# Kernel tuning notes

Measured on AMD Instinct MI355X. Metric: run time of the kernel, lower is better.

The kernel has to match this reference:

```python
import jax, jax.numpy as jnp
import numpy as np

N_HEAD = 16


def setup_inputs() -> dict:
    key = jax.random.key(0)
    ks = jax.random.split(key, 5)
    B, S, D = 4, 2048, 1024
    scale = 1.0 / np.sqrt(D)
    return {
        "x": jax.random.normal(ks[0], (B, S, D), dtype=jnp.float32),
        "Wq": jax.random.normal(ks[1], (D, D), dtype=jnp.float32) * scale,
        "bq": jnp.zeros((D,), dtype=jnp.float32),
        "Wk": jax.random.normal(ks[2], (D, D), dtype=jnp.float32) * scale,
        "bk": jnp.zeros((D,), dtype=jnp.float32),
        "Wv": jax.random.normal(ks[3], (D, D), dtype=jnp.float32) * scale,
        "bv": jnp.zeros((D,), dtype=jnp.float32),
        "Wo": jax.random.normal(ks[4], (D, D), dtype=jnp.float32) * scale,
        "bo": jnp.zeros((D,), dtype=jnp.float32),
    }


def reference(x, Wq, bq, Wk, bk, Wv, bv, Wo, bo):
    B, S, D = x.shape
    H = N_HEAD
    Dh = D // H
    # projections (torch Linear == x @ W^T + b; here W stored as (in, out))
    q = (x @ Wq + bq).reshape(B, S, H, Dh).transpose(0, 2, 1, 3)  # (B,H,S,Dh)
    k = (x @ Wk + bk).reshape(B, S, H, Dh).transpose(0, 2, 1, 3)
    v = (x @ Wv + bv).reshape(B, S, H, Dh).transpose(0, 2, 1, 3)
    scores = jnp.einsum("bhsd,bhtd->bhst", q, k) / jnp.sqrt(jnp.float32(Dh))
    causal = jnp.tril(jnp.ones((S, S), dtype=bool))  # (S,S)
    scores = jnp.where(causal[None, None], scores, -jnp.inf)
    weights = jax.nn.softmax(scores, axis=-1)  # (B,H,S,S)
    attn = jnp.einsum("bhst,bhtd->bhsd", weights, v)
    attn = attn.transpose(0, 2, 1, 3).reshape(B, S, D)
    out = attn @ Wo + bo
    return out
```

## Files before the change

kernel.cpp:

```cpp
#include <hip/hip_runtime.h>
#include <hip/hip_bf16.h>


typedef __bf16 bf16x8 __attribute__((ext_vector_type(8)));
typedef float f32x4 __attribute__((ext_vector_type(4)));
typedef unsigned short u16;

__device__ __forceinline__ u16 f2b(float f) {
    __hip_bfloat16 h = __float2bfloat16(f);
    return __builtin_bit_cast(unsigned short, h);
}

__device__ __forceinline__ f32x4 mfma16(bf16x8 a, bf16x8 b, f32x4 c) {
    return __builtin_amdgcn_mfma_f32_16x16x32_bf16(a, b, c, 0, 0, 0);
}

typedef const __attribute__((address_space(1))) unsigned int* gas1_t;
typedef __attribute__((address_space(3))) unsigned int* las3_t;
__device__ __forceinline__ void gld16(const void* g, void* l) {
    __builtin_amdgcn_global_load_lds((gas1_t)g, (las3_t)l, 16, 0, 0);
}

__global__ __launch_bounds__(256) void convert_x(const float* __restrict__ x,
                                                 u16* __restrict__ xb, int n4) {
    int i = blockIdx.x * 256 + threadIdx.x;
    if (i < n4) {
        float4 v = ((const float4*)x)[i];
        ushort4 u;
        u.x = f2b(v.x); u.y = f2b(v.y); u.z = f2b(v.z); u.w = f2b(v.w);
        ((ushort4*)xb)[i] = u;
    }
}

__global__ __launch_bounds__(256) void transpose_w(const float* __restrict__ Wq,
                                                   const float* __restrict__ Wk,
                                                   const float* __restrict__ Wv,
                                                   const float* __restrict__ Wo,
                                                   u16* __restrict__ wqkvt,
                                                   u16* __restrict__ wot) {
    const int z = blockIdx.z;
    const float* src = (z == 0) ? Wq : (z == 1) ? Wk : (z == 2) ? Wv : Wo;
    u16* dst = (z == 3) ? wot : (wqkvt + (size_t)z * 1024 * 1024);
    __shared__ float tile[32][33];
    const int tx = threadIdx.x, ty = threadIdx.y;
    const int nbase = blockIdx.x * 32, kbase = blockIdx.y * 32;
    for (int j = 0; j < 4; ++j)
        tile[ty + j * 8][tx] = src[(size_t)(kbase + ty + j * 8) * 1024 + nbase + tx];
    __syncthreads();
    for (int j = 0; j < 4; ++j)
        dst[(size_t)(nbase + ty + j * 8) * 1024 + kbase + tx] = f2b(tile[tx][ty + j * 8]);
}

__global__ __launch_bounds__(256) void pack_bqkv(const float* __restrict__ bq,
                                                 const float* __restrict__ bk,
                                                 const float* __restrict__ bv,
                                                 float* __restrict__ bqkv) {
    int i = blockIdx.x * 256 + threadIdx.x;
    bqkv[i] = (i < 1024) ? bq[i] : (i < 2048) ? bk[i - 1024] : bv[i - 2048];
}

template <int MODE>
__global__ __launch_bounds__(256) void gemm_bt(const u16* __restrict__ A,
                                               const u16* __restrict__ Bt,
                                               const float* __restrict__ bias,
                                               void* __restrict__ Cout,
                                               void* __restrict__ Cout2,
                                               int M, int N, int K, int ldc) {
    const int tid = threadIdx.x;
    const int l = tid & 63;
    const int w = tid >> 6;
    const int tileM = blockIdx.x * 128;
    const int tileN = blockIdx.y * 128;

    __shared__ u16 As[128 * 32];
    __shared__ u16 Bs[128 * 32];

    const int srow = l >> 2;
    const int schunk = l & 3;
    const int mrow = l & 15;
    const int g8 = (l >> 4) * 8;
    const int waveM = (w & 1) * 64;
    const int waveN = (w >> 1) * 64;

    f32x4 acc[4][4] = {};

    for (int k0 = 0; k0 < K; k0 += 32) {
        gld16(A + (size_t)(tileM + w * 32 + srow) * K + k0 + schunk * 8, &As[(w * 2) * 512]);
        gld16(A + (size_t)(tileM + w * 32 + 16 + srow) * K + k0 + schunk * 8, &As[(w * 2 + 1) * 512]);
        gld16(Bt + (size_t)(tileN + w * 32 + srow) * K + k0 + schunk * 8, &Bs[(w * 2) * 512]);
        gld16(Bt + (size_t)(tileN + w * 32 + 16 + srow) * K + k0 + schunk * 8, &Bs[(w * 2 + 1) * 512]);
        __syncthreads();

        bf16x8 af[4], bf[4];
        for (int im = 0; im < 4; ++im)
            af[im] = *(const bf16x8*)&As[(waveM + im * 16 + mrow) * 32 + g8];
        for (int in = 0; in < 4; ++in)
            bf[in] = *(const bf16x8*)&Bs[(waveN + in * 16 + mrow) * 32 + g8];
        for (int im = 0; im < 4; ++im)
            for (int in = 0; in < 4; ++in)
                acc[im][in] = mfma16(af[im], bf[in], acc[im][in]);
        __syncthreads();
    }

    const int rbase = (l >> 4) * 4;
    for (int im = 0; im < 4; ++im) {
        for (int in = 0; in < 4; ++in) {
            const int gm0 = tileM + waveM + im * 16 + rbase;
            const int gn = tileN + waveN + in * 16 + (l & 15);
            const float bv_ = bias[gn];
            if (MODE == 1) {
                float* out = (float*)Cout;
                for (int r = 0; r < 4; ++r)
                    out[(size_t)(gm0 + r) * ldc + gn] = acc[im][in][r] + bv_;
            } else if (tileN < 2048) {
                const float qs = (tileN < 1024) ? 0.125f * 1.4426950408889634f : 1.0f;
                u16* out = (u16*)Cout;
                for (int r = 0; r < 4; ++r)
                    out[(size_t)(gm0 + r) * 2048 + gn] = f2b((acc[im][in][r] + bv_) * qs);
            } else {
                u16* out = (u16*)Cout2;
                const int b = gm0 >> 11, s0 = gm0 & 2047;
                const int gn2 = gn - 2048;
                const int h = gn2 >> 6, dh = gn2 & 63;
                ushort4 u;
                u.x = f2b(acc[im][in][0] + bv_);
                u.y = f2b(acc[im][in][1] + bv_);
                u.z = f2b(acc[im][in][2] + bv_);
                u.w = f2b(acc[im][in][3] + bv_);
                *(ushort4*)&out[((size_t)((b * 16 + h) * 64 + dh)) * 2048 + s0] = u;
            }
        }
    }
}

__global__ __launch_bounds__(256, 2) void attn_kernel(const u16* __restrict__ qk,
                                                      const u16* __restrict__ vt,
                                                      u16* __restrict__ attn) {
    const int bh = blockIdx.x;
    const int qt = 15 - (int)blockIdx.y;
    const int b = bh >> 4, h = bh & 15;
    const int q0 = qt * 128;
    const int tid = threadIdx.x, l = tid & 63, w = tid >> 6;
    const int q = l & 15;
    const int g = l >> 4;
    const int g8 = g * 8;

    __shared__ u16 Ks[64 * 72];
    __shared__ u16 Vs[64 * 72];
    __shared__ u16 Ps[128 * 72];

    const int srow = tid >> 3, sch = tid & 7;
    const u16* kgb = qk + (size_t)(b * 2048 + srow) * 2048 + 1024 + h * 64 + sch * 8;
    const u16* vgb = vt + (size_t)(bh * 64 + srow) * 2048 + sch * 8;

    for (int i = 0; i < 4; ++i) {
        const int idx = i * 256 + tid;
        const int row = idx >> 3, ch = idx & 7;
        *(uint4*)&Ps[row * 72 + ch * 8] =
            *(const uint4*)&qk[(size_t)(b * 2048 + q0 + row) * 2048 + h * 64 + ch * 8];
    }
    __syncthreads();
    bf16x8 qb[2][2];
    for (int c = 0; c < 2; ++c) {
        qb[c][0] = *(const bf16x8*)&Ps[(w * 32 + c * 16 + q) * 72 + g8];
        qb[c][1] = *(const bf16x8*)&Ps[(w * 32 + c * 16 + q) * 72 + 32 + g8];
    }

    float li[2] = {0.f, 0.f};
    f32x4 o[2][4] = {};
    const int tmax = 2 * qt + 1;
    const int tdiag = (q0 + w * 32 + 31) >> 6;

    uint4 kreg[2], vreg[2];
    for (int j = 0; j < 2; ++j) {
        kreg[j] = *(const uint4*)(kgb + (size_t)(j * 32) * 2048);
        vreg[j] = *(const uint4*)(vgb + (size_t)(j * 32) * 2048);
    }

    for (int t = 0; t <= tmax; ++t) {
        __syncthreads();
        for (int j = 0; j < 2; ++j) {
            *(uint4*)&Ks[(srow + j * 32) * 72 + sch * 8] = kreg[j];
            *(uint4*)&Vs[(srow + j * 32) * 72 + sch * 8] = vreg[j];
        }
        __syncthreads();
        if (t < tmax) {
            for (int j = 0; j < 2; ++j) {
                kreg[j] = *(const uint4*)(kgb + (size_t)((t + 1) * 64 + j * 32) * 2048);
                vreg[j] = *(const uint4*)(vgb + (size_t)(j * 32) * 2048 + (t + 1) * 64);
            }
        }
        if (t > tdiag) continue;
        const int kv0 = t * 64;

        f32x4 st[2][4] = {};
        for (int kh = 0; kh < 2; ++kh)
            for (int cb = 0; cb < 4; ++cb) {
                bf16x8 ka = *(const bf16x8*)&Ks[(cb * 16 + q) * 72 + kh * 32 + g8];
                st[0][cb] = mfma16(ka, qb[0][kh], st[0][cb]);
                st[1][cb] = mfma16(ka, qb[1][kh], st[1][cb]);
            }
        for (int c = 0; c < 2; ++c) {
            if (t == tdiag) {
                const int qg = q0 + w * 32 + c * 16 + q;
                for (int cb = 0; cb < 4; ++cb)
                    for (int r = 0; r < 4; ++r) {
                        const int key = kv0 + cb * 16 + g * 4 + r;
                        if (key > qg) st[c][cb][r] = -1e30f;
                    }
            }
            float ps = 0.f;
            for (int cb = 0; cb < 4; ++cb)
                for (int r = 0; r < 4; ++r) {
                    const float p = __builtin_amdgcn_exp2f(st[c][cb][r]);
                    st[c][cb][r] = p;
                    ps += p;
                }
            li[c] += ps;
            for (int cb = 0; cb < 4; ++cb) {
                ushort4 u;
                u.x = f2b(st[c][cb][0]); u.y = f2b(st[c][cb][1]);
                u.z = f2b(st[c][cb][2]); u.w = f2b(st[c][cb][3]);
                *(ushort4*)&Ps[(w * 32 + c * 16 + q) * 72 + cb * 16 + g * 4] = u;
            }
        }
        __builtin_amdgcn_s_waitcnt(0xC07F);
        for (int kh = 0; kh < 2; ++kh) {
            bf16x8 pb0 = *(const bf16x8*)&Ps[(w * 32 + q) * 72 + kh * 32 + g8];
            bf16x8 pb1 = *(const bf16x8*)&Ps[(w * 32 + 16 + q) * 72 + kh * 32 + g8];
            for (int cb = 0; cb < 4; ++cb) {
                bf16x8 va = *(const bf16x8*)&Vs[(cb * 16 + q) * 72 + kh * 32 + g8];
                o[0][cb] = mfma16(va, pb0, o[0][cb]);
                o[1][cb] = mfma16(va, pb1, o[1][cb]);
            }
        }
    }

    for (int c = 0; c < 2; ++c) {
        float ps = li[c];
        ps += __shfl_xor(ps, 16);
        ps += __shfl_xor(ps, 32);
        const float inv = 1.0f / ps;
        const size_t tok = (size_t)(b * 2048 + q0 + w * 32 + c * 16 + q);
        for (int cb = 0; cb < 4; ++cb) {
            ushort4 u;
            u.x = f2b(o[c][cb][0] * inv); u.y = f2b(o[c][cb][1] * inv);
            u.z = f2b(o[c][cb][2] * inv); u.w = f2b(o[c][cb][3] * inv);
            *(ushort4*)&attn[tok * 1024 + h * 64 + cb * 16 + g * 4] = u;
        }
    }
}

extern "C" void kernel_launch(void* const* d_in, const int* in_sizes, int n_in,
                              void* d_out, int out_size, void* d_ws, size_t ws_size,
                              hipStream_t stream) {
    const float* x  = (const float*)d_in[0];
    const float* Wq = (const float*)d_in[1];
    const float* bq = (const float*)d_in[2];
    const float* Wk = (const float*)d_in[3];
    const float* bk = (const float*)d_in[4];
    const float* Wv = (const float*)d_in[5];
    const float* bv = (const float*)d_in[6];
    const float* Wo = (const float*)d_in[7];
    const float* bo = (const float*)d_in[8];
    float* out = (float*)d_out;

    char* ws = (char*)d_ws;
    size_t off = 0;
    auto alloc = [&](size_t bytes) -> void* {
        void* p = ws + off;
        off += (bytes + 255) & ~(size_t)255;
        return p;
    };
    u16*   xb    = (u16*)alloc(8192ull * 1024 * 2);
    u16*   wqkvt = (u16*)alloc(3072ull * 1024 * 2);
    u16*   wot   = (u16*)alloc(1024ull * 1024 * 2);
    float* bqkv  = (float*)alloc(3072ull * 4);
    u16*   qk    = (u16*)alloc(8192ull * 2048 * 2);
    u16*   vt    = (u16*)alloc(8192ull * 1024 * 2);
    u16*   attn  = (u16*)alloc(8192ull * 1024 * 2);

    convert_x<<<8192, 256, 0, stream>>>(x, xb, 8192 * 1024 / 4);
    transpose_w<<<dim3(32, 32, 4), dim3(32, 8), 0, stream>>>(Wq, Wk, Wv, Wo, wqkvt, wot);
    pack_bqkv<<<12, 256, 0, stream>>>(bq, bk, bv, bqkv);
    gemm_bt<0><<<dim3(64, 24), 256, 0, stream>>>(xb, wqkvt, bqkv, qk, vt, 8192, 3072, 1024, 0);
    attn_kernel<<<dim3(64, 16), 256, 0, stream>>>(qk, vt, attn);
    gemm_bt<1><<<dim3(64, 8), 256, 0, stream>>>(attn, wot, bo, out, nullptr, 8192, 1024, 1024, 1024);
}
```

Baseline: 296.3 us.

## Double-buffer K/V tiles in LDS via direct global-to-LDS loads with XOR swizzle

Replaces the register-staged K/V tile loads with global_load_lds directly into double-buffered shared memory. The next tile is prefetched while the current one is computed, which cuts the loop to one barrier per iteration. An XOR swizzle on the 64-wide rows replaces the padded layout to avoid bank conflicts. It raises LDS use and relies on the barrier to make the asynchronous LDS writes visible.

```diff
diff --git a/kernel.cpp b/kernel.cpp
--- a/kernel.cpp
+++ b/kernel.cpp
@@ -145,13 +145,14 @@
     const int g = l >> 4;
     const int g8 = g * 8;
 
-    __shared__ u16 Ks[64 * 72];
-    __shared__ u16 Vs[64 * 72];
+    __shared__ u16 Ks[2][64 * 64];
+    __shared__ u16 Vs[2][64 * 64];
     __shared__ u16 Ps[128 * 72];
 
-    const int srow = tid >> 3, sch = tid & 7;
-    const u16* kgb = qk + (size_t)(b * 2048 + srow) * 2048 + 1024 + h * 64 + sch * 8;
-    const u16* vgb = vt + (size_t)(bh * 64 + srow) * 2048 + sch * 8;
+    const int sr8 = l >> 3;
+    const int gc = (l & 7) ^ sr8;
+    const u16* kgl = qk + (size_t)(b * 2048 + w * 16 + sr8) * 2048 + 1024 + h * 64 + gc * 8;
+    const u16* vgl = vt + (size_t)(bh * 64 + w * 16 + sr8) * 2048 + gc * 8;
 
     for (int i = 0; i < 4; ++i) {
         const int idx = i * 256 + tid;
@@ -159,81 +160,88 @@
         *(uint4*)&Ps[row * 72 + ch * 8] =
             *(const uint4*)&qk[(size_t)(b * 2048 + q0 + row) * 2048 + h * 64 + ch * 8];
     }
+    for (int j = 0; j < 2; ++j) {
+        gld16(kgl + (size_t)(j * 8) * 2048, &Ks[0][(w * 16 + j * 8) * 64]);
+        gld16(vgl + (size_t)(j * 8) * 2048, &Vs[0][(w * 16 + j * 8) * 64]);
+    }
     __syncthreads();
+
     bf16x8 qb[2][2];
     for (int c = 0; c < 2; ++c) {
         qb[c][0] = *(const bf16x8*)&Ps[(w * 32 + c * 16 + q) * 72 + g8];
         qb[c][1] = *(const bf16x8*)&Ps[(w * 32 + c * 16 + q) * 72 + 32 + g8];
     }
 
+    const int cl0 = ((g) ^ (q & 7)) * 8;
+    const int cl1 = ((4 + g) ^ (q & 7)) * 8;
+
     float li[2] = {0.f, 0.f};
     f32x4 o[2][4] = {};
     const int tmax = 2 * qt + 1;
     const int tdiag = (q0 + w * 32 + 31) >> 6;
 
-    uint4 kreg[2], vreg[2];
-    for (int j = 0; j < 2; ++j) {
-        kreg[j] = *(const uint4*)(kgb + (size_t)(j * 32) * 2048);
-        vreg[j] = *(const uint4*)(vgb + (size_t)(j * 32) * 2048);
-    }
-
     for (int t = 0; t <= tmax; ++t) {
-        __syncthreads();
+        const int tp = (t < tmax) ? t + 1 : tmax;
+        const int nb = (t + 1) & 1;
         for (int j = 0; j < 2; ++j) {
-            *(uint4*)&Ks[(srow + j * 32) * 72 + sch * 8] = kreg[j];
-            *(uint4*)&Vs[(srow + j * 32) * 72 + sch * 8] = vreg[j];
-        }
-        __syncthreads();
-        if (t < tmax) {
-            for (int j = 0; j < 2; ++j) {
-                kreg[j] = *(const uint4*)(kgb + (size_t)((t + 1) * 64 + j * 32) * 2048);
-                vreg[j] = *(const uint4*)(vgb + (size_t)(j * 32) * 2048 + (t + 1) * 64);
-            }
-        }
-        if (t > tdiag) continue;
-        const int kv0 = t * 64;
-
-        f32x4 st[2][4] = {};
-        for (int kh = 0; kh < 2; ++kh)
+            gld16(kgl + (size_t)(tp * 64 + j * 8) * 2048, &Ks[nb][(w * 16 + j * 8) * 64]);
+            gld16(vgl + (size_t)(j * 8) * 2048 + tp * 64, &Vs[nb][(w * 16 + j * 8) * 64]);
+        }
+
+        if (t <= tdiag) {
+            const int cb0 = t & 1;
+            const int kv0 = t * 64;
+            const u16* ks = &Ks[cb0][0];
+            const u16* vs = &Vs[cb0][0];
+
+            f32x4 st[2][4] = {};
             for (int cb = 0; cb < 4; ++cb) {
-                bf16x8 ka = *(const bf16x8*)&Ks[(cb * 16 + q) * 72 + kh * 32 + g8];
-                st[0][cb] = mfma16(ka, qb[0][kh], st[0][cb]);
-                st[1][cb] = mfma16(ka, qb[1][kh], st[1][cb]);
-            }
-        for (int c = 0; c < 2; ++c) {
-            if (t == tdiag) {
-                const int qg = q0 + w * 32 + c * 16 + q;
+                bf16x8 ka0 = *(const bf16x8*)&ks[(cb * 16 + q) * 64 + cl0];
+                bf16x8 ka1 = *(const bf16x8*)&ks[(cb * 16 + q) * 64 + cl1];
+                st[0][cb] = mfma16(ka0, qb[0][0], st[0][cb]);
+                st[1][cb] = mfma16(ka0, qb[1][0], st[1][cb]);
+                st[0][cb] = mfma16(ka1, qb[0][1], st[0][cb]);
+                st[1][cb] = mfma16(ka1, qb[1][1], st[1][cb]);
+            }
+            for (int c = 0; c < 2; ++c) {
+                if (t == tdiag) {
+                    const int qg = q0 + w * 32 + c * 16 + q;
+                    for (int cb = 0; cb < 4; ++cb)
+                        for (int r = 0; r < 4; ++r) {
+                            const int key = kv0 + cb * 16 + g * 4 + r;
+                            if (key > qg) st[c][cb][r] = -1e30f;
+                        }
+                }
+                float ps = 0.f;
                 for (int cb = 0; cb < 4; ++cb)
                     for (int r = 0; r < 4; ++r) {
-                        const int key = kv0 + cb * 16 + g * 4 + r;
-                        if (key > qg) st[c][cb][r] = -1e30f;
+                        const float p = __builtin_amdgcn_exp2f(st[c][cb][r]);
+                        st[c][cb][r] = p;
+                        ps += p;
                     }
-            }
-            float ps = 0.f;
-            for (int cb = 0; cb < 4; ++cb)
-                for (int r = 0; r < 4; ++r) {
-                    const float p = __builtin_amdgcn_exp2f(st[c][cb][r]);
-                    st[c][cb][r] = p;
-                    ps += p;
+                li[c] += ps;
+                for (int cb = 0; cb < 4; ++cb) {
+                    ushort4 u;
+                    u.x = f2b(st[c][cb][0]); u.y = f2b(st[c][cb][1]);
+                    u.z = f2b(st[c][cb][2]); u.w = f2b(st[c][cb][3]);
+                    *(ushort4*)&Ps[(w * 32 + c * 16 + q) * 72 + cb * 16 + g * 4] = u;
                 }
-            li[c] += ps;
+            }
+            __builtin_amdgcn_s_waitcnt(0xC07F);
             for (int cb = 0; cb < 4; ++cb) {
-                ushort4 u;
-                u.x = f2b(st[c][cb][0]); u.y = f2b(st[c][cb][1]);
-                u.z = f2b(st[c][cb][2]); u.w = f2b(st[c][cb][3]);
-                *(ushort4*)&Ps[(w * 32 + c * 16 + q) * 72 + cb * 16 + g * 4] = u;
-            }
-        }
-        __builtin_amdgcn_s_waitcnt(0xC07F);
-        for (int kh = 0; kh < 2; ++kh) {
-            bf16x8 pb0 = *(const bf16x8*)&Ps[(w * 32 + q) * 72 + kh * 32 + g8];
-            bf16x8 pb1 = *(const bf16x8*)&Ps[(w * 32 + 16 + q) * 72 + kh * 32 + g8];
-            for (int cb = 0; cb < 4; ++cb) {
-                bf16x8 va = *(const bf16x8*)&Vs[(cb * 16 + q) * 72 + kh * 32 + g8];
-                o[0][cb] = mfma16(va, pb0, o[0][cb]);
-                o[1][cb] = mfma16(va, pb1, o[1][cb]);
-            }
-        }
+                bf16x8 va0 = *(const bf16x8*)&vs[(cb * 16 + q) * 64 + cl0];
+                bf16x8 va1 = *(const bf16x8*)&vs[(cb * 16 + q) * 64 + cl1];
+                bf16x8 pb00 = *(const bf16x8*)&Ps[(w * 32 + q) * 72 + g8];
+                bf16x8 pb01 = *(const bf16x8*)&Ps[(w * 32 + q) * 72 + 32 + g8];
+                bf16x8 pb10 = *(const bf16x8*)&Ps[(w * 32 + 16 + q) * 72 + g8];
+                bf16x8 pb11 = *(const bf16x8*)&Ps[(w * 32 + 16 + q) * 72 + 32 + g8];
+                o[0][cb] = mfma16(va0, pb00, o[0][cb]);
+                o[1][cb] = mfma16(va0, pb10, o[1][cb]);
+                o[0][cb] = mfma16(va1, pb01, o[0][cb]);
+                o[1][cb] = mfma16(va1, pb11, o[1][cb]);
+            }
+        }
+        __syncthreads();
     }
 
     for (int c = 0; c < 2; ++c) {
```

Result: faster. 256.7 us (-13.4%).
